# Optimization experiments

Measured on AMD Instinct MI355X. Metric: run time of the kernel, lower is better.

The kernel has to match this reference:

```python
import jax, jax.numpy as jnp
import numpy as np

EPS = 1e-5

def conv1d(x, w, b, pad):
    # x: [B,C_in,S], w: [C_out,C_in,K] -> [B,C_out,S]
    y = jax.lax.conv_general_dilated(x, w, window_strides=(1,), padding=[(pad, pad)],
                                     dimension_numbers=('NCH', 'OIH', 'NCH'))
    return y + b[None, :, None]

def bn(x, gamma, beta, mean, var):
    # inference-mode BatchNorm1d over channel dim of [B,C,S]
    scale = gamma * jax.lax.rsqrt(var + EPS)
    shift = beta - mean * scale
    return x * scale[None, :, None] + shift[None, :, None]

def setup_inputs() -> dict:
    key = jax.random.key(0)
    ks = jax.random.split(key, 16)
    B, S, D, C, K = 32, 2048, 128, 256, 5
    x = jax.random.normal(ks[0], (B, S, D), dtype=jnp.float32)
    start_padding_indices = jax.random.randint(ks[1], (B,), 0, S, dtype=jnp.int64 if jax.config.jax_enable_x64 else jnp.int32)
    def conv_init(k, co, ci, kk):
        fan = ci * kk
        return jax.random.normal(k, (co, ci, kk), dtype=jnp.float32) / np.sqrt(fan)
    W1 = conv_init(ks[2], C, D, K); b1 = jnp.zeros((C,), jnp.float32)
    g1 = jnp.ones((C,), jnp.float32); be1 = jnp.zeros((C,), jnp.float32)
    m1 = jax.random.normal(ks[3], (C,), dtype=jnp.float32) * 0.1
    v1 = jax.random.uniform(ks[4], (C,), dtype=jnp.float32, minval=0.5, maxval=1.5)
    W2 = conv_init(ks[5], C, C, K); b2 = jnp.zeros((C,), jnp.float32)
    g2 = jnp.ones((C,), jnp.float32); be2 = jnp.zeros((C,), jnp.float32)
    m2 = jax.random.normal(ks[6], (C,), dtype=jnp.float32) * 0.1
    v2 = jax.random.uniform(ks[7], (C,), dtype=jnp.float32, minval=0.5, maxval=1.5)
    Wf = conv_init(ks[8], D, C, 1); bf = jnp.zeros((D,), jnp.float32)
    return {"x": x, "start_padding_indices": start_padding_indices,
            "W1": W1, "b1": b1, "g1": g1, "be1": be1, "m1": m1, "v1": v1,
            "W2": W2, "b2": b2, "g2": g2, "be2": be2, "m2": m2, "v2": v2,
            "Wf": Wf, "bf": bf}

def reference(x, start_padding_indices, W1, b1, g1, be1, m1, v1,
              W2, b2, g2, be2, m2, v2, Wf, bf):
    B, S, D = x.shape
    K = W1.shape[-1]
    h = jnp.transpose(x, (0, 2, 1))                      # [B,D,S]
    h = jax.nn.relu(bn(conv1d(h, W1, b1, K // 2), g1, be1, m1, v1))
    h = jax.nn.relu(bn(conv1d(h, W2, b2, K // 2), g2, be2, m2, v2))
    h = conv1d(h, Wf, bf, 0)                             # [B,D,S]
    conv_out = jnp.transpose(h, (0, 2, 1))               # [B,S,D]
    # vectorized masked mean: -1 sentinel -> full length; 0 -> zeros
    lengths = jnp.where(start_padding_indices == -1, S, start_padding_indices)  # [B]
    mask = jnp.arange(S)[None, :] < lengths[:, None]     # [B,S]
    sums = jnp.sum(conv_out * mask[:, :, None].astype(conv_out.dtype), axis=1)  # [B,D]
    denom = jnp.maximum(lengths, 1).astype(conv_out.dtype)[:, None]
    pooled = jnp.where(lengths[:, None] > 0, sums / denom, jnp.zeros_like(sums))
    return pooled
```

## Files before the change

### kernel.cpp

```cpp
#include <hip/hip_runtime.h>

#define S_LEN 2048
#define NBATCH 32

typedef __bf16 bf16x8 __attribute__((ext_vector_type(8)));
typedef float f32x4 __attribute__((ext_vector_type(4)));
typedef unsigned short bf_t;

__device__ __forceinline__ unsigned short f2bf(float f) {
  __bf16 h = (__bf16)f;
  return __builtin_bit_cast(unsigned short, h);
}

#if __has_builtin(__builtin_amdgcn_global_load_lds)
#define USE_GLL 1
#else
#define USE_GLL 0
#endif

__device__ __forceinline__ void load_lds16(const void* g, void* ldsbase) {
#if USE_GLL
  __builtin_amdgcn_global_load_lds(
      (const __attribute__((address_space(1))) unsigned int*)g,
      (__attribute__((address_space(3))) unsigned int*)ldsbase, 16, 0, 0);
#else
  *(int4*)((char*)ldsbase + (threadIdx.x & 63) * 16) =
      *(const int4*)((const char*)g);
#endif
}

#define WAITV8  asm volatile("s_waitcnt vmcnt(8)" ::: "memory")
#define WAITV0  asm volatile("s_waitcnt vmcnt(0)" ::: "memory")

__global__ void convert_x(const float* __restrict__ x, bf_t* __restrict__ xb) {
  const size_t i = (size_t)blockIdx.x * blockDim.x + threadIdx.x;
  const float4 a = ((const float4*)x)[2 * i];
  const float4 c = ((const float4*)x)[2 * i + 1];
  ushort4 o0; o0.x = f2bf(a.x); o0.y = f2bf(a.y); o0.z = f2bf(a.z); o0.w = f2bf(a.w);
  ushort4 o1; o1.x = f2bf(c.x); o1.y = f2bf(c.y); o1.z = f2bf(c.z); o1.w = f2bf(c.w);
  ((ushort4*)xb)[2 * i] = o0;
  ((ushort4*)xb)[2 * i + 1] = o1;
}

__global__ void fold_bn(const float* __restrict__ b1, const float* __restrict__ g1,
                        const float* __restrict__ be1, const float* __restrict__ m1,
                        const float* __restrict__ v1,
                        const float* __restrict__ b2, const float* __restrict__ g2,
                        const float* __restrict__ be2, const float* __restrict__ m2,
                        const float* __restrict__ v2, float* __restrict__ abuf,
                        float* __restrict__ zp) {
  int c = threadIdx.x;
  if (c < 64) zp[c] = 0.f;
  if (c < 256) {
    float a1 = g1[c] * rsqrtf(v1[c] + 1e-5f);
    abuf[c] = a1;
    abuf[256 + c] = (b1[c] - m1[c]) * a1 + be1[c];
    float a2 = g2[c] * rsqrtf(v2[c] + 1e-5f);
    abuf[512 + c] = a2;
    abuf[768 + c] = (b2[c] - m2[c]) * a2 + be2[c];
  }
}

template <int CIN, int TAPS>
__global__ void prep_w2(const float* __restrict__ w, bf_t* __restrict__ wfm) {
  const int idx = blockIdx.x * 256 + threadIdx.x;
  constexpr int total = 256 * CIN * TAPS;
  if (idx >= total) return;
  const int j = idx & 7;
  const int l = (idx >> 3) & 63;
  const int f = (idx >> 9) & 7;
  const int wr = (idx >> 12) & 1;
  const int tg = idx >> 13;
  const int co = wr * 128 + f * 16 + (l & 15);
  const int cc = tg / (TAPS * 4);
  const int k = (tg / 4) % TAPS;
  const int q = tg & 3;
  const int ci = cc * 128 + q * 32 + (l >> 4) * 8 + j;
  wfm[idx] = f2bf(w[((size_t)co * CIN + ci) * TAPS + k]);
}

template <int CIN, int COUT, int TAPS>
__global__ void prep_w(const float* __restrict__ w, bf_t* __restrict__ wfm) {
  constexpr int T = CIN * TAPS / 32;
  const int idx = blockIdx.x * 256 + threadIdx.x;
  constexpr int total = COUT * CIN * TAPS;
  if (idx >= total) return;
  const int j = idx & 7;
  const int l = (idx >> 3) & 63;
  const int f = (idx >> 9) & 3;
  const int gt = idx >> 11;
  const int t = gt % T;
  const int g = gt / T;
  const int co = g * 64 + f * 16 + (l & 15);
  const int cc = t / (TAPS * 4);
  const int k = (t / 4) % TAPS;
  const int q = t & 3;
  const int ci = cc * 128 + q * 32 + (l >> 4) * 8 + j;
  wfm[idx] = f2bf(w[((size_t)co * CIN + ci) * TAPS + k]);
}

template <int CIN, int TAPS>
__device__ __forceinline__ void conv_body(
    const bf_t* __restrict__ xin, const bf_t* __restrict__ wfm,
    const float* __restrict__ alpha, const float* __restrict__ bias,
    const float* __restrict__ zp, bf_t* __restrict__ hout) {
  constexpr int HALO = (TAPS - 1) / 2;
  constexpr int P = (CIN / 128) * TAPS * 4;
  constexpr int NKT = P / 2;

  __shared__ char smem[131072];

  const int tid = threadIdx.x;
  const int l = tid & 63;
  const int wv = tid >> 6;
  const int wr = wv >> 2;
  const int wn = wv & 3;
  const int b = blockIdx.x >> 3;
  const int s0 = (blockIdx.x & 7) << 8;
  const int l15 = l & 15;
  const int l4 = l >> 4;
  const int wu16 = (tid - l) * 16;

  f32x4 acc[8][4] = {};
  bf16x8 afr[2][8];
  bf16x8 bfr01[2], bfr23[2];

  auto STAGE_A = [&](int jt, int sub) {
    const char* src = (const char*)wfm + (size_t)(2 * jt + sub) * 16384;
    char* dst = smem + (jt & 1) * 32768 + sub * 16384;
    load_lds16(src + tid * 16, dst + wu16);
    load_lds16(src + 8192 + tid * 16, dst + 8192 + wu16);
  };

  auto STAGE_B = [&](int jt, int sub) {
    const int t = 2 * jt + sub;
    const int cc = t / (TAPS * 4);
    const int k = (t >> 2) % TAPS;
    const int q = t & 3;
    char* dst = smem + 65536 + (jt & 1) * 32768 + sub * 16384;
    const int r0 = tid >> 2;
    const int slot = ((r0 & 3) ^ ((r0 >> 2) & 3)) << 4;
    const char* srcb = (const char*)xin +
        ((size_t)b * S_LEN * CIN + cc * 128 + q * 32) * 2 +
        (((tid & 3) * 16) ^ slot);
    {
      const int s = s0 + r0 - HALO + k;
      const char* src = ((unsigned)s < (unsigned)S_LEN)
          ? srcb + (size_t)s * (CIN * 2) : ((const char*)zp + (((tid & 3) * 16) ^ slot));
      load_lds16(src, dst + wu16);
    }
    {
      const int s = s0 + r0 + 128 - HALO + k;
      const char* src = ((unsigned)s < (unsigned)S_LEN)
          ? srcb + (size_t)s * (CIN * 2) : ((const char*)zp + (((tid & 3) * 16) ^ slot));
      load_lds16(src, dst + 8192 + wu16);
    }
  };

  auto LDB = [&](const char* Bb, int sub, int r) -> bf16x8 {
    const int slot = (((r & 3) ^ ((r >> 2) & 3)) << 4);
    return *(const bf16x8*)(Bb + sub * 16384 + r * 64 + ((l4 * 16) ^ slot));
  };

  STAGE_A(0, 0); STAGE_B(0, 0); STAGE_A(0, 1); STAGE_B(0, 1);
  STAGE_A(1, 0); STAGE_B(1, 0); STAGE_A(1, 1);
  WAITV8;
  __builtin_amdgcn_s_barrier();

  {
    const char* Ab0 = smem;
    const char* Bb0 = smem + 65536;
#pragma unroll
    for (int f = 0; f < 8; ++f)
      afr[0][f] = *(const bf16x8*)(Ab0 + wr * 8192 + f * 1024 + l * 16);
    bfr01[0] = LDB(Bb0, 0, wn * 64 + 0 + l15);
    bfr01[1] = LDB(Bb0, 0, wn * 64 + 16 + l15);
  }

#pragma unroll 1
  for (int j = 0; j < NKT; ++j) {
    const char* Ab = smem + (j & 1) * 32768;
    const char* Bb = smem + 65536 + (j & 1) * 32768;
    const char* Abn = smem + ((j + 1) & 1) * 32768;
    const char* Bbn = smem + 65536 + ((j + 1) & 1) * 32768;

    bfr23[0] = LDB(Bb, 0, wn * 64 + 32 + l15);
    bfr23[1] = LDB(Bb, 0, wn * 64 + 48 + l15);
    if (j + 1 < NKT) STAGE_B(j + 1, 1);
    __builtin_amdgcn_s_setprio(1);
#pragma unroll
    for (int f = 0; f < 8; ++f) {
      acc[f][0] = __builtin_amdgcn_mfma_f32_16x16x32_bf16(afr[0][f], bfr01[0], acc[f][0], 0, 0, 0);
      acc[f][1] = __builtin_amdgcn_mfma_f32_16x16x32_bf16(afr[0][f], bfr01[1], acc[f][1], 0, 0, 0);
    }
    __builtin_amdgcn_s_setprio(0);
    WAITV8;
    __builtin_amdgcn_s_barrier();
    __builtin_amdgcn_sched_barrier(0);

#pragma unroll
    for (int f = 0; f < 8; ++f)
      afr[1][f] = *(const bf16x8*)(Ab + 16384 + wr * 8192 + f * 1024 + l * 16);
    bfr01[0] = LDB(Bb, 1, wn * 64 + 0 + l15);
    bfr01[1] = LDB(Bb, 1, wn * 64 + 16 + l15);
    if (j + 2 < NKT) STAGE_A(j + 2, 0);
    __builtin_amdgcn_s_setprio(1);
#pragma unroll
    for (int f = 0; f < 8; ++f) {
      acc[f][2] = __builtin_amdgcn_mfma_f32_16x16x32_bf16(afr[0][f], bfr23[0], acc[f][2], 0, 0, 0);
      acc[f][3] = __builtin_amdgcn_mfma_f32_16x16x32_bf16(afr[0][f], bfr23[1], acc[f][3], 0, 0, 0);
    }
    __builtin_amdgcn_s_setprio(0);
    __builtin_amdgcn_s_barrier();
    __builtin_amdgcn_sched_barrier(0);

    bfr23[0] = LDB(Bb, 1, wn * 64 + 32 + l15);
    bfr23[1] = LDB(Bb, 1, wn * 64 + 48 + l15);
    if (j + 2 < NKT) STAGE_B(j + 2, 0);
    __builtin_amdgcn_s_setprio(1);
#pragma unroll
    for (int f = 0; f < 8; ++f) {
      acc[f][0] = __builtin_amdgcn_mfma_f32_16x16x32_bf16(afr[1][f], bfr01[0], acc[f][0], 0, 0, 0);
      acc[f][1] = __builtin_amdgcn_mfma_f32_16x16x32_bf16(afr[1][f], bfr01[1], acc[f][1], 0, 0, 0);
    }
    __builtin_amdgcn_s_setprio(0);
    WAITV8;
    __builtin_amdgcn_s_barrier();
    __builtin_amdgcn_sched_barrier(0);

    if (j + 1 < NKT) {
#pragma unroll
      for (int f = 0; f < 8; ++f)
        afr[0][f] = *(const bf16x8*)(Abn + wr * 8192 + f * 1024 + l * 16);
      bfr01[0] = LDB(Bbn, 0, wn * 64 + 0 + l15);
      bfr01[1] = LDB(Bbn, 0, wn * 64 + 16 + l15);
    }
    if (j + 2 < NKT) STAGE_A(j + 2, 1);
    __builtin_amdgcn_s_setprio(1);
#pragma unroll
    for (int f = 0; f < 8; ++f) {
      acc[f][2] = __builtin_amdgcn_mfma_f32_16x16x32_bf16(afr[1][f], bfr23[0], acc[f][2], 0, 0, 0);
      acc[f][3] = __builtin_amdgcn_mfma_f32_16x16x32_bf16(afr[1][f], bfr23[1], acc[f][3], 0, 0, 0);
    }
    __builtin_amdgcn_s_setprio(0);
    __builtin_amdgcn_s_barrier();
    __builtin_amdgcn_sched_barrier(0);
  }

  WAITV0;
  __syncthreads();
  const int cobase = wr * 128;
#pragma unroll
  for (int f = 0; f < 8; ++f) {
    const int co0 = cobase + f * 16 + l4 * 4;
    const f32x4 al = *(const f32x4*)(alpha + co0);
    const f32x4 bi = *(const f32x4*)(bias + co0);
#pragma unroll
    for (int n = 0; n < 4; ++n) {
      const int sp = wn * 64 + n * 16 + l15;
      ushort4 pk;
      pk.x = f2bf(fmaxf(acc[f][n][0] * al[0] + bi[0], 0.f));
      pk.y = f2bf(fmaxf(acc[f][n][1] * al[1] + bi[1], 0.f));
      pk.z = f2bf(fmaxf(acc[f][n][2] * al[2] + bi[2], 0.f));
      pk.w = f2bf(fmaxf(acc[f][n][3] * al[3] + bi[3], 0.f));
      *(ushort4*)(smem + sp * 512 + ((co0 * 2) ^ ((sp & 7) << 4))) = pk;
    }
  }
  __syncthreads();
  {
    char* hb = (char*)hout + ((size_t)(b * S_LEN + s0) * 256) * 2;
#pragma unroll
    for (int k = 0; k < 16; ++k) {
      const int c = tid + k * 512;
      const int sp = c >> 5;
      const int col = (c & 31) * 16;
      const int4 v = *(const int4*)(smem + sp * 512 + (col ^ ((sp & 7) << 4)));
      *(int4*)(hb + (size_t)sp * 512 + col) = v;
    }
  }
}

__global__ __launch_bounds__(512, 2)
void conv_gemm_L1(const bf_t* __restrict__ xin, const bf_t* __restrict__ wfm,
                  const float* __restrict__ alpha, const float* __restrict__ bias,
                  const float* __restrict__ zp, bf_t* __restrict__ hout) {
  conv_body<128, 5>(xin, wfm, alpha, bias, zp, hout);
}

__global__ __launch_bounds__(512, 2)
void conv_gemm_L2(const bf_t* __restrict__ xin, const bf_t* __restrict__ wfm,
                  const float* __restrict__ alpha, const float* __restrict__ bias,
                  const float* __restrict__ zp, bf_t* __restrict__ hout) {
  conv_body<256, 5>(xin, wfm, alpha, bias, zp, hout);
}

__global__ __launch_bounds__(512, 4)
void conv_pool(const bf_t* __restrict__ xin, const bf_t* __restrict__ wfm,
               const float* __restrict__ bfin, const int* __restrict__ spi,
               float* __restrict__ gpart) {
  constexpr int CIN = 256;
  constexpr int T = 8;

  __shared__ char smem[128 * 256];
  __shared__ float red[4][128];

  const int tid = threadIdx.x;
  const int l = tid & 63;
  const int wv = tid >> 6;
  const int wr = wv >> 2;
  const int wn = wv & 3;
  const int nb = blockIdx.x;
  const int b = nb >> 4;
  const int st = nb & 15;
  const int s0 = st << 7;
  const int l15 = l & 15;
  const int l4 = l >> 4;

  f32x4 acc[4][2] = {};
  const bf_t* wbase = wfm + (size_t)wr * (T * 2048);

  for (int cc = 0; cc < 2; ++cc) {
    const char* src = (const char*)xin + ((size_t)b * S_LEN * CIN + cc * 128) * 2;
    for (int off = tid * 16; off < 128 * 256; off += 512 * 16) {
      const int row = off >> 8;
      const int c = off & 255;
      const int cs = c ^ ((row & 7) << 4);
      void* ldsbase = (void*)(smem + (off - l * 16));
      load_lds16(src + (size_t)(s0 + row) * (CIN * 2) + cs, ldsbase);
    }
    __syncthreads();

#pragma unroll
    for (int q = 0; q < 4; ++q) {
      const int t = cc * 4 + q;
      bf16x8 bfr[2];
#pragma unroll
      for (int fn = 0; fn < 2; ++fn) {
        const int row = wn * 32 + fn * 16 + l15;
        const int cb = q * 64 + l4 * 16;
        bfr[fn] = *(const bf16x8*)(smem + row * 256 + (cb ^ ((row & 7) << 4)));
      }
#pragma unroll
      for (int f = 0; f < 4; ++f) {
        const bf16x8 afr =
            *(const bf16x8*)(wbase + ((size_t)(t * 4 + f) * 64 + l) * 8);
        acc[f][0] = __builtin_amdgcn_mfma_f32_16x16x32_bf16(afr, bfr[0], acc[f][0], 0, 0, 0);
        acc[f][1] = __builtin_amdgcn_mfma_f32_16x16x32_bf16(afr, bfr[1], acc[f][1], 0, 0, 0);
      }
    }
    __syncthreads();
  }

  int len = spi[b];
  if (len < 0) len = S_LEN;

#pragma unroll
  for (int f = 0; f < 4; ++f) {
    const int co0 = wr * 64 + f * 16 + l4 * 4;
    const f32x4 bi = *(const f32x4*)(bfin + co0);
    f32x4 vs = {};
#pragma unroll
    for (int fn = 0; fn < 2; ++fn) {
      const int s = s0 + wn * 32 + fn * 16 + l15;
      const float m = (s < len) ? 1.f : 0.f;
      vs[0] += (acc[f][fn][0] + bi[0]) * m;
      vs[1] += (acc[f][fn][1] + bi[1]) * m;
      vs[2] += (acc[f][fn][2] + bi[2]) * m;
      vs[3] += (acc[f][fn][3] + bi[3]) * m;
    }
#pragma unroll
    for (int d = 1; d < 16; d <<= 1) {
      vs[0] += __shfl_xor(vs[0], d, 64);
      vs[1] += __shfl_xor(vs[1], d, 64);
      vs[2] += __shfl_xor(vs[2], d, 64);
      vs[3] += __shfl_xor(vs[3], d, 64);
    }
    if (l15 == 0) {
      red[wn][co0 + 0] = vs[0];
      red[wn][co0 + 1] = vs[1];
      red[wn][co0 + 2] = vs[2];
      red[wn][co0 + 3] = vs[3];
    }
  }
  __syncthreads();
  if (tid < 128) {
    float p = red[0][tid] + red[1][tid] + red[2][tid] + red[3][tid];
    gpart[((size_t)b * 16 + st) * 128 + tid] = p;
  }
}

__global__ void finalize(const float* __restrict__ gpart, const int* __restrict__ spi,
                         float* __restrict__ out) {
  const int b = blockIdx.x;
  const int d = threadIdx.x;
  float s = 0.f;
#pragma unroll
  for (int t = 0; t < 16; ++t) s += gpart[((size_t)b * 16 + t) * 128 + d];
  int len = spi[b];
  if (len < 0) len = S_LEN;
  float denom = (float)(len < 1 ? 1 : len);
  out[b * 128 + d] = s / denom;
}

extern "C" void kernel_launch(void* const* d_in, const int* in_sizes, int n_in,
                              void* d_out, int out_size, void* d_ws, size_t ws_size,
                              hipStream_t stream) {
  (void)in_sizes; (void)n_in; (void)out_size; (void)ws_size;
  const float* x = (const float*)d_in[0];
  const int* spi = (const int*)d_in[1];
  const float* W1 = (const float*)d_in[2];
  const float* b1 = (const float*)d_in[3];
  const float* g1 = (const float*)d_in[4];
  const float* be1 = (const float*)d_in[5];
  const float* m1 = (const float*)d_in[6];
  const float* v1 = (const float*)d_in[7];
  const float* W2 = (const float*)d_in[8];
  const float* b2 = (const float*)d_in[9];
  const float* g2 = (const float*)d_in[10];
  const float* be2 = (const float*)d_in[11];
  const float* m2 = (const float*)d_in[12];
  const float* v2 = (const float*)d_in[13];
  const float* Wf = (const float*)d_in[14];
  const float* bf_ = (const float*)d_in[15];
  float* out = (float*)d_out;

  char* ws = (char*)d_ws;
  float* zp   = (float*)(ws);
  bf_t* xb    = (bf_t*)(ws + 4096);
  bf_t* h1    = (bf_t*)(ws + 16781312);
  bf_t* h2    = (bf_t*)(ws + 50335744);
  bf_t* wf1   = (bf_t*)(ws + 83890176);
  bf_t* wf2   = (bf_t*)(ws + 84217856);
  bf_t* wff   = (bf_t*)(ws + 84873216);
  float* abuf = (float*)(ws + 84938752);
  float* gpart= (float*)(ws + 84942848);

  convert_x<<<4096, 256, 0, stream>>>(x, xb);
  fold_bn<<<1, 256, 0, stream>>>(b1, g1, be1, m1, v1, b2, g2, be2, m2, v2, abuf, zp);
  prep_w2<128, 5><<<640, 256, 0, stream>>>(W1, wf1);
  prep_w2<256, 5><<<1280, 256, 0, stream>>>(W2, wf2);
  prep_w<256, 128, 1><<<128, 256, 0, stream>>>(Wf, wff);

  conv_gemm_L1<<<256, 512, 0, stream>>>(xb, wf1, abuf, abuf + 256, zp, h1);
  conv_gemm_L2<<<256, 512, 0, stream>>>(h1, wf2, abuf + 512, abuf + 768, zp, h2);
  conv_pool<<<512, 512, 0, stream>>>(h2, wff, bf_, spi, gpart);
  finalize<<<32, 128, 0, stream>>>(gpart, spi, out);
}
```

Measured before the change: 104.2 us.

## Restructure conv GEMM main loop into two half-tile stages with simpler prefetch

Replaces the four-phase ping-pong loop, which held register-prefetched A/B fragments across barriers, with two per-subtile phases. Each phase loads its whole A and B fragment set from LDS, issues the next global-to-LDS stage, then runs all 32 MFMAs. The prologue now waits for the first stage fully, and the vmcnt waits are adjusted near the loop tail. This cuts register pressure and barrier count, but LDS read latency is no longer hidden behind MFMAs from the previous phase.

After: 104.6 us. Within noise of the previous version (+0.4%).

```diff
diff --git a/kernel.cpp b/kernel.cpp
--- a/kernel.cpp
+++ b/kernel.cpp
@@ -30,6 +30,7 @@
 }
 
 #define WAITV8  asm volatile("s_waitcnt vmcnt(8)" ::: "memory")
+#define WAITV4  asm volatile("s_waitcnt vmcnt(4)" ::: "memory")
 #define WAITV0  asm volatile("s_waitcnt vmcnt(0)" ::: "memory")
 
 __global__ void convert_x(const float* __restrict__ x, bf_t* __restrict__ xb) {
@@ -122,8 +123,6 @@
   const int wu16 = (tid - l) * 16;
 
   f32x4 acc[8][4] = {};
-  bf16x8 afr[2][8];
-  bf16x8 bfr01[2], bfr23[2];
 
   auto STAGE_A = [&](int jt, int sub) {
     const char* src = (const char*)wfm + (size_t)(2 * jt + sub) * 16384;
@@ -162,89 +161,59 @@
     return *(const bf16x8*)(Bb + sub * 16384 + r * 64 + ((l4 * 16) ^ slot));
   };
 
-  STAGE_A(0, 0); STAGE_B(0, 0); STAGE_A(0, 1); STAGE_B(0, 1);
-  STAGE_A(1, 0); STAGE_B(1, 0); STAGE_A(1, 1);
-  WAITV8;
+  STAGE_A(0, 0); STAGE_A(0, 1); STAGE_B(0, 0); STAGE_B(0, 1);
+  WAITV0;
+  STAGE_A(1, 0); STAGE_B(1, 0);
   __builtin_amdgcn_s_barrier();
-
-  {
-    const char* Ab0 = smem;
-    const char* Bb0 = smem + 65536;
-#pragma unroll
-    for (int f = 0; f < 8; ++f)
-      afr[0][f] = *(const bf16x8*)(Ab0 + wr * 8192 + f * 1024 + l * 16);
-    bfr01[0] = LDB(Bb0, 0, wn * 64 + 0 + l15);
-    bfr01[1] = LDB(Bb0, 0, wn * 64 + 16 + l15);
-  }
 
 #pragma unroll 1
   for (int j = 0; j < NKT; ++j) {
     const char* Ab = smem + (j & 1) * 32768;
     const char* Bb = smem + 65536 + (j & 1) * 32768;
-    const char* Abn = smem + ((j + 1) & 1) * 32768;
-    const char* Bbn = smem + 65536 + ((j + 1) & 1) * 32768;
-
-    bfr23[0] = LDB(Bb, 0, wn * 64 + 32 + l15);
-    bfr23[1] = LDB(Bb, 0, wn * 64 + 48 + l15);
-    if (j + 1 < NKT) STAGE_B(j + 1, 1);
-    __builtin_amdgcn_s_setprio(1);
-#pragma unroll
-    for (int f = 0; f < 8; ++f) {
-      acc[f][0] = __builtin_amdgcn_mfma_f32_16x16x32_bf16(afr[0][f], bfr01[0], acc[f][0], 0, 0, 0);
-      acc[f][1] = __builtin_amdgcn_mfma_f32_16x16x32_bf16(afr[0][f], bfr01[1], acc[f][1], 0, 0, 0);
-    }
-    __builtin_amdgcn_s_setprio(0);
-    WAITV8;
-    __builtin_amdgcn_s_barrier();
-    __builtin_amdgcn_sched_barrier(0);
-
-#pragma unroll
-    for (int f = 0; f < 8; ++f)
-      afr[1][f] = *(const bf16x8*)(Ab + 16384 + wr * 8192 + f * 1024 + l * 16);
-    bfr01[0] = LDB(Bb, 1, wn * 64 + 0 + l15);
-    bfr01[1] = LDB(Bb, 1, wn * 64 + 16 + l15);
-    if (j + 2 < NKT) STAGE_A(j + 2, 0);
-    __builtin_amdgcn_s_setprio(1);
-#pragma unroll
-    for (int f = 0; f < 8; ++f) {
-      acc[f][2] = __builtin_amdgcn_mfma_f32_16x16x32_bf16(afr[0][f], bfr23[0], acc[f][2], 0, 0, 0);
-      acc[f][3] = __builtin_amdgcn_mfma_f32_16x16x32_bf16(afr[0][f], bfr23[1], acc[f][3], 0, 0, 0);
-    }
-    __builtin_amdgcn_s_setprio(0);
-    __builtin_amdgcn_s_barrier();
-    __builtin_amdgcn_sched_barrier(0);
-
-    bfr23[0] = LDB(Bb, 1, wn * 64 + 32 + l15);
-    bfr23[1] = LDB(Bb, 1, wn * 64 + 48 + l15);
-    if (j + 2 < NKT) STAGE_B(j + 2, 0);
-    __builtin_amdgcn_s_setprio(1);
-#pragma unroll
-    for (int f = 0; f < 8; ++f) {
-      acc[f][0] = __builtin_amdgcn_mfma_f32_16x16x32_bf16(afr[1][f], bfr01[0], acc[f][0], 0, 0, 0);
-      acc[f][1] = __builtin_amdgcn_mfma_f32_16x16x32_bf16(afr[1][f], bfr01[1], acc[f][1], 0, 0, 0);
-    }
-    __builtin_amdgcn_s_setprio(0);
-    WAITV8;
-    __builtin_amdgcn_s_barrier();
-    __builtin_amdgcn_sched_barrier(0);
-
-    if (j + 1 < NKT) {
+
+    {
+      __builtin_amdgcn_s_setprio(1);
+      bf16x8 afr[8], bfr[4];
 #pragma unroll
       for (int f = 0; f < 8; ++f)
-        afr[0][f] = *(const bf16x8*)(Abn + wr * 8192 + f * 1024 + l * 16);
-      bfr01[0] = LDB(Bbn, 0, wn * 64 + 0 + l15);
-      bfr01[1] = LDB(Bbn, 0, wn * 64 + 16 + l15);
-    }
-    if (j + 2 < NKT) STAGE_A(j + 2, 1);
-    __builtin_amdgcn_s_setprio(1);
-#pragma unroll
-    for (int f = 0; f < 8; ++f) {
-      acc[f][2] = __builtin_amdgcn_mfma_f32_16x16x32_bf16(afr[1][f], bfr23[0], acc[f][2], 0, 0, 0);
-      acc[f][3] = __builtin_amdgcn_mfma_f32_16x16x32_bf16(afr[1][f], bfr23[1], acc[f][3], 0, 0, 0);
-    }
-    __builtin_amdgcn_s_setprio(0);
-    __builtin_amdgcn_s_barrier();
-    __builtin_amdgcn_sched_barrier(0);
+        afr[f] = *(const bf16x8*)(Ab + wr * 8192 + f * 1024 + l * 16);
+#pragma unroll
+      for (int n = 0; n < 4; ++n)
+        bfr[n] = LDB(Bb, 0, wn * 64 + n * 16 + l15);
+      if (j + 1 < NKT) { STAGE_B(j + 1, 1); STAGE_A(j + 1, 1); }
+#pragma unroll
+      for (int f = 0; f < 8; ++f)
+#pragma unroll
+        for (int n = 0; n < 4; ++n)
+          acc[f][n] = __builtin_amdgcn_mfma_f32_16x16x32_bf16(
+              afr[f], bfr[n], acc[f][n], 0, 0, 0);
+      __builtin_amdgcn_s_setprio(0);
+      if (j < NKT - 1) { WAITV8; } else { WAITV0; }
+      __builtin_amdgcn_s_barrier();
+      __builtin_amdgcn_sched_barrier(0);
+    }
+
+    {
+      __builtin_amdgcn_s_setprio(1);
+      bf16x8 afr[8], bfr[4];
+#pragma unroll
+      for (int f = 0; f < 8; ++f)
+        afr[f] = *(const bf16x8*)(Ab + 16384 + wr * 8192 + f * 1024 + l * 16);
+#pragma unroll
+      for (int n = 0; n < 4; ++n)
+        bfr[n] = LDB(Bb, 1, wn * 64 + n * 16 + l15);
+      if (j + 2 < NKT) { STAGE_A(j + 2, 0); STAGE_B(j + 2, 0); }
+#pragma unroll
+      for (int f = 0; f < 8; ++f)
+#pragma unroll
+        for (int n = 0; n < 4; ++n)
+          acc[f][n] = __builtin_amdgcn_mfma_f32_16x16x32_bf16(
+              afr[f], bfr[n], acc[f][n], 0, 0, 0);
+      __builtin_amdgcn_s_setprio(0);
+      if (j <= NKT - 3) { WAITV8; } else if (j == NKT - 2) { WAITV4; }
+      __builtin_amdgcn_s_barrier();
+      __builtin_amdgcn_sched_barrier(0);
+    }
   }
 
   WAITV0;
```
